# Kernel tuning notes

Measured on AMD Instinct MI355X. Metric: run time of the kernel, lower is better.

## Reference

```python
import jax, jax.numpy as jnp
import numpy as np

N_NODES = 50000


def _gcn_conv(x, W, b, src, dst, n):
    # PyG GCNConv: linear, then D^{-1/2}(A+I)D^{-1/2} aggregation, then bias.
    x = x @ W  # [N, out]
    loops = jnp.arange(n, dtype=src.dtype)
    src_f = jnp.concatenate([src, loops])  # add self-loops
    dst_f = jnp.concatenate([dst, loops])
    deg = jax.ops.segment_sum(jnp.ones_like(dst_f, dtype=x.dtype), dst_f, num_segments=n)
    dinv = jnp.where(deg > 0, jax.lax.rsqrt(deg), 0.0)
    norm = dinv[src_f] * dinv[dst_f]            # [E+N]
    msg = x[src_f] * norm[:, None]              # gather + scale
    out = jax.ops.segment_sum(msg, dst_f, num_segments=n)  # scatter-add
    return out + b


def setup_inputs() -> dict:
    key = jax.random.key(0)
    k1, k2, k3, k4 = jax.random.split(key, 4)
    ninp = 128
    emb = jax.random.normal(k1, (N_NODES, ninp), dtype=jnp.float32)
    emb = emb.at[0].set(0.0)  # padding_idx=0
    W1 = jax.random.normal(k2, (ninp, 2 * ninp), dtype=jnp.float32) * (1.0 / np.sqrt(ninp))
    b1 = jnp.zeros((2 * ninp,), dtype=jnp.float32)
    W2 = jax.random.normal(k3, (2 * ninp, ninp), dtype=jnp.float32) * (1.0 / np.sqrt(2 * ninp))
    b2 = jnp.zeros((ninp,), dtype=jnp.float32)
    edge_index = jax.random.randint(k4, (2, 800000), 0, N_NODES, dtype=jnp.int64)
    return {"emb": emb, "W1": W1, "b1": b1, "W2": W2, "b2": b2, "edge_index": edge_index}


def reference(emb, W1, b1, W2, b2, edge_index) -> jnp.ndarray:
    src, dst = edge_index[0], edge_index[1]
    h = _gcn_conv(emb, W1, b1, src, dst, N_NODES)   # [N, 2*ninp]
    # dropout in eval mode -> identity
    out = _gcn_conv(h, W2, b2, src, dst, N_NODES)   # [N, ninp]
    return out
```

## Files before the change

kernel.cpp:

```cpp
#include <hip/hip_runtime.h>

#define N_NODES 50000
#define N_EDGES 800000
#define NB 196

typedef unsigned int uint;
typedef short bf16x8 __attribute__((ext_vector_type(8)));
typedef float f32x4 __attribute__((ext_vector_type(4)));
typedef uint uint4v __attribute__((ext_vector_type(4)));

__device__ __forceinline__ ushort f2bf(float f) {
    union { float f; uint u; } v; v.f = f;
    uint r = (v.u + 0x7FFFu + ((v.u >> 16) & 1u)) >> 16;
    return (ushort)r;
}
__device__ __forceinline__ float bf_lo(uint u) { return __uint_as_float(u << 16); }
__device__ __forceinline__ float bf_hi(uint u) { return __uint_as_float(u & 0xFFFF0000u); }

__global__ void k_prep(const float* __restrict__ emb, const float* __restrict__ W1,
                       const float* __restrict__ W2, const float* __restrict__ b1,
                       uint* __restrict__ emb_h, ushort* __restrict__ W12t,
                       float* __restrict__ bvec, int* __restrict__ counts) {
    int b = blockIdx.x;
    int tid = threadIdx.x;
    if (b < 3125) {
        int t = b * 256 + tid;
        const float4* i4 = (const float4*)emb + (size_t)t * 2;
        float4 v0 = i4[0], v1 = i4[1];
        uint4 o;
        o.x = (uint)f2bf(v0.x) | ((uint)f2bf(v0.y) << 16);
        o.y = (uint)f2bf(v0.z) | ((uint)f2bf(v0.w) << 16);
        o.z = (uint)f2bf(v1.x) | ((uint)f2bf(v1.y) << 16);
        o.w = (uint)f2bf(v1.z) | ((uint)f2bf(v1.w) << 16);
        ((uint4*)emb_h)[t] = o;
    } else if (b < 3125 + NB) {
        int i = (b - 3125) * 256 + tid;
        if (i < N_NODES) counts[i] = 0;
    } else {
        int k = (b - (3125 + NB)) * 2 + (tid >> 7);
        int n = tid & 127;
        float s = 0.f;
        if (k < 128) {
            for (int m = 0; m < 256; ++m) s = fmaf(W1[(size_t)k * 256 + m], W2[(size_t)m * 128 + n], s);
            W12t[(size_t)n * 128 + k] = f2bf(s);
        } else if (k == 128) {
            for (int m = 0; m < 256; ++m) s = fmaf(b1[m], W2[(size_t)m * 128 + n], s);
            bvec[n] = s;
        }
    }
}


__global__ void k_histrank(const int* __restrict__ dst, int* __restrict__ counts,
                           ushort* __restrict__ rank) {
    int e = blockIdx.x * 256 + threadIdx.x;
    if (e < N_EDGES) rank[e] = (ushort)atomicAdd(&counts[dst[e]], 1);
}

__global__ void k_blocksum(const int* __restrict__ counts, int* __restrict__ bsum) {
    __shared__ int lds[256];
    int t = threadIdx.x;
    int i = blockIdx.x * 256 + t;
    int v = (i < N_NODES) ? counts[i] : 0;
    lds[t] = v;
    __syncthreads();
    for (int off = 128; off > 0; off >>= 1) {
        if (t < off) lds[t] += lds[t + off];
        __syncthreads();
    }
    if (t == 0) bsum[blockIdx.x] = lds[0];
}

__global__ void k_scanb(const int* __restrict__ bsum, int* __restrict__ boff) {
    __shared__ int lds[256];
    int t = threadIdx.x;
    int v = (t < NB) ? bsum[t] : 0;
    lds[t] = v;
    __syncthreads();
    for (int off = 1; off < 256; off <<= 1) {
        int o = (t >= off) ? lds[t - off] : 0;
        __syncthreads();
        lds[t] += o;
        __syncthreads();
    }
    if (t < NB) boff[t] = lds[t] - v;
}

__global__ void k_scatter_rp(const int* __restrict__ counts, const int* __restrict__ boff,
                             int* __restrict__ row_ptr, float* __restrict__ dinv) {
    __shared__ int lds[256];
    int t = threadIdx.x;
    int i = blockIdx.x * 256 + t;
    int v = (i < N_NODES) ? counts[i] : 0;
    lds[t] = v;
    __syncthreads();
    for (int off = 1; off < 256; off <<= 1) {
        int o = (t >= off) ? lds[t - off] : 0;
        __syncthreads();
        lds[t] += o;
        __syncthreads();
    }
    if (i < N_NODES) {
        row_ptr[i] = boff[blockIdx.x] + lds[t] - v;
        dinv[i] = rsqrtf((float)(v + 1));
    }
    if (i == 0) row_ptr[N_NODES] = N_EDGES;
}

__global__ void k_fillr(const int* __restrict__ src, const int* __restrict__ dst,
                        const ushort* __restrict__ rank, const int* __restrict__ row_ptr,
                        const float* __restrict__ dinv, uint* __restrict__ csr) {
    int e = blockIdx.x * 256 + threadIdx.x;
    if (e >= N_EDGES) return;
    int s = src[e];
    int pos = row_ptr[dst[e]] + (int)rank[e];
    csr[pos] = ((uint)s << 16) | (uint)f2bf(dinv[s]);
}

__device__ __forceinline__ void gather_core(const uint* __restrict__ xh,
                                            const uint* __restrict__ csr,
                                            int beg, int end, int node, float dd,
                                            int q, int fl, float o[8], float& scn) {
    const uint4* xb = (const uint4*)xh;
    float a[8];
    #pragma unroll
    for (int i = 0; i < 8; ++i) a[i] = 0.f;
    float sc = 0.f;

    for (int j = beg + q; j < end; j += 32) {
        uint e0 = csr[j];
        uint def = e0 & 0xFFFF0000u;
        uint e[8];
        e[0] = e0;
        #pragma unroll
        for (int i = 1; i < 8; ++i) {
            int ji = j + 4 * i;
            e[i] = (ji < end) ? csr[ji] : def;
        }
        uint4 u[8];
        #pragma unroll
        for (int i = 0; i < 8; ++i) u[i] = xb[(size_t)(e[i] >> 16) * 16 + fl];
        #pragma unroll
        for (int i = 0; i < 8; ++i) {
            float c = bf_lo(e[i]);
            sc += c;
            a[0] = fmaf(c, bf_lo(u[i].x), a[0]); a[1] = fmaf(c, bf_hi(u[i].x), a[1]);
            a[2] = fmaf(c, bf_lo(u[i].y), a[2]); a[3] = fmaf(c, bf_hi(u[i].y), a[3]);
            a[4] = fmaf(c, bf_lo(u[i].z), a[4]); a[5] = fmaf(c, bf_hi(u[i].z), a[5]);
            a[6] = fmaf(c, bf_lo(u[i].w), a[6]); a[7] = fmaf(c, bf_hi(u[i].w), a[7]);
        }
    }
    #pragma unroll
    for (int off = 16; off < 64; off <<= 1) {
        #pragma unroll
        for (int i = 0; i < 8; ++i) a[i] += __shfl_xor(a[i], off);
        sc += __shfl_xor(sc, off);
    }
    float dd2 = dd * dd;
    const uint4* xs = (const uint4*)xh + (size_t)node * 16 + fl;
    uint4 u = *xs;
    float s[8] = { bf_lo(u.x), bf_hi(u.x), bf_lo(u.y), bf_hi(u.y),
                   bf_lo(u.z), bf_hi(u.z), bf_lo(u.w), bf_hi(u.w) };
    #pragma unroll
    for (int i = 0; i < 8; ++i) o[i] = fmaf(dd, a[i], dd2 * s[i]);
    scn = fmaf(dd, sc, dd2);
}

__global__ void k_gather1(const uint* __restrict__ xh, const uint* __restrict__ csr,
                          const int* __restrict__ rp, const float* __restrict__ dinv,
                          uint* __restrict__ outp) {
    int node = blockIdx.x * 4 + (threadIdx.x >> 6);
    int lane = threadIdx.x & 63;
    int q = lane >> 4, fl = lane & 15;
    int beg = rp[node], end = rp[node + 1];
    float o[8], scn;
    gather_core(xh, csr, beg, end, node, dinv[node], q, fl, o, scn);
    if (q == 0) {
        uint4v p;
        p.x = (uint)f2bf(o[0]) | ((uint)f2bf(o[1]) << 16);
        p.y = (uint)f2bf(o[2]) | ((uint)f2bf(o[3]) << 16);
        p.z = (uint)f2bf(o[4]) | ((uint)f2bf(o[5]) << 16);
        p.w = (uint)f2bf(o[6]) | ((uint)f2bf(o[7]) << 16);
        __builtin_nontemporal_store(p, (uint4v*)outp + (size_t)node * 16 + fl);
    }
}

__global__ void __launch_bounds__(1024)
k_gather_gemm(const uint* __restrict__ xh, const uint* __restrict__ csr,
              const int* __restrict__ rp, const float* __restrict__ dinv,
              const ushort* __restrict__ Wt, const float* __restrict__ bvec,
              const float* __restrict__ b2, float* __restrict__ out) {
    __shared__ ushort rows[16 * 128];
    __shared__ float nvl[16];
    const int w = threadIdx.x >> 6;
    const int lane = threadIdx.x & 63;
    const int node = blockIdx.x * 16 + w;
    const int q = lane >> 4, fl = lane & 15;
    const int beg = rp[node], end = rp[node + 1];

    float o[8], scn;
    gather_core(xh, csr, beg, end, node, dinv[node], q, fl, o, scn);
    if (q == 0) {
        uint4 p;
        p.x = (uint)f2bf(o[0]) | ((uint)f2bf(o[1]) << 16);
        p.y = (uint)f2bf(o[2]) | ((uint)f2bf(o[3]) << 16);
        p.z = (uint)f2bf(o[4]) | ((uint)f2bf(o[5]) << 16);
        p.w = (uint)f2bf(o[6]) | ((uint)f2bf(o[7]) << 16);
        int idx = (w * 128 + fl * 8) ^ ((w & 7) << 3);
        *(uint4*)&rows[idx] = p;
        if (fl == 0) nvl[w] = scn;
    }
    __syncthreads();

    if (w < 8) {
        const int col = w * 16 + (lane & 15);
        const int ksub = (lane >> 4) * 8;
        const int row = lane & 15;
        f32x4 acc = (f32x4){0.f, 0.f, 0.f, 0.f};
        #pragma unroll
        for (int kc = 0; kc < 4; ++kc) {
            int idxr = (row * 128 + kc * 32 + ksub) ^ ((row & 7) << 3);
            bf16x8 af = *(const bf16x8*)&rows[idxr];
            bf16x8 bf = *(const bf16x8*)(Wt + (size_t)col * 128 + kc * 32 + ksub);
            acc = __builtin_amdgcn_mfma_f32_16x16x32_bf16(af, bf, acc, 0, 0, 0);
        }
        const int rb = (lane >> 4) * 4;
        float bv = bvec[col], bb = b2[col];
        #pragma unroll
        for (int e = 0; e < 4; ++e) {
            float nv = nvl[rb + e];
            out[(size_t)(blockIdx.x * 16 + rb + e) * 128 + col] = acc[e] + nv * bv + bb;
        }
    }
}

extern "C" void kernel_launch(void* const* d_in, const int* in_sizes, int n_in,
                              void* d_out, int out_size, void* d_ws, size_t ws_size,
                              hipStream_t stream) {
    const float* emb = (const float*)d_in[0];
    const float* W1  = (const float*)d_in[1];
    const float* b1  = (const float*)d_in[2];
    const float* W2  = (const float*)d_in[3];
    const float* b2  = (const float*)d_in[4];
    const int*   ei  = (const int*)d_in[5];
    const int* src = ei;
    const int* dst = ei + N_EDGES;

    char* ws = (char*)d_ws;
    float*  dinv    = (float*) (ws);
    int*    counts  = (int*)   (ws + (256ull << 10));
    int*    row_ptr = (int*)   (ws + (512ull << 10));
    int*    bsum    = (int*)   (ws + (768ull << 10));
    int*    boff    = (int*)   (ws + (772ull << 10));
    ushort* rank    = (ushort*)(ws + (1ull << 20));
    uint*   csr     = (uint*)  (ws + (3ull << 20));
    ushort* W12t    = (ushort*)(ws + (6656ull << 10));
    float*  bvec    = (float*) (ws + (6720ull << 10));
    uint*   emb_h   = (uint*)  (ws + (7ull  << 20));
    uint*   G       = (uint*)  (ws + (20ull << 20));
    float*  out     = (float*)d_out;

    k_prep<<<3386, 256, 0, stream>>>(emb, W1, W2, b1, emb_h, W12t, bvec, counts);

    k_histrank<<<(N_EDGES + 255) / 256, 256, 0, stream>>>(dst, counts, rank);
    k_blocksum<<<NB, 256, 0, stream>>>(counts, bsum);
    k_scanb<<<1, 256, 0, stream>>>(bsum, boff);
    k_scatter_rp<<<NB, 256, 0, stream>>>(counts, boff, row_ptr, dinv);
    k_fillr<<<(N_EDGES + 255) / 256, 256, 0, stream>>>(src, dst, rank, row_ptr, dinv, csr);

    k_gather1<<<12500, 256, 0, stream>>>(emb_h, csr, row_ptr, dinv, G);
    k_gather_gemm<<<3125, 1024, 0, stream>>>(G, csr, row_ptr, dinv,
                                             (const ushort*)W12t, bvec, b2, out);
}
```

Baseline: 171.5 us.

## Split fused second gather+GEMM into separate gather and MFMA GEMM kernels

Replaces the fused 1024-thread gather+GEMM kernel with a 256-thread gather kernel that writes bf16 aggregated rows and a per-node scale to workspace, followed by a separate MFMA GEMM kernel. The aim is to free the gather from the block-wide barrier and idle waves of the fused kernel, which should improve occupancy. It also marks CSR loads as nontemporal. The cost is an extra kernel launch and an extra round trip of the intermediate through global memory.

```diff
diff --git a/kernel.cpp b/kernel.cpp
--- a/kernel.cpp
+++ b/kernel.cpp
@@ -128,14 +128,14 @@
     float sc = 0.f;
 
     for (int j = beg + q; j < end; j += 32) {
-        uint e0 = csr[j];
+        uint e0 = __builtin_nontemporal_load(&csr[j]);
         uint def = e0 & 0xFFFF0000u;
         uint e[8];
         e[0] = e0;
         #pragma unroll
         for (int i = 1; i < 8; ++i) {
             int ji = j + 4 * i;
-            e[i] = (ji < end) ? csr[ji] : def;
+            e[i] = (ji < end) ? __builtin_nontemporal_load(&csr[ji]) : def;
         }
         uint4 u[8];
         #pragma unroll
@@ -185,51 +185,64 @@
     }
 }
 
-__global__ void __launch_bounds__(1024)
-k_gather_gemm(const uint* __restrict__ xh, const uint* __restrict__ csr,
-              const int* __restrict__ rp, const float* __restrict__ dinv,
-              const ushort* __restrict__ Wt, const float* __restrict__ bvec,
-              const float* __restrict__ b2, float* __restrict__ out) {
-    __shared__ ushort rows[16 * 128];
-    __shared__ float nvl[16];
-    const int w = threadIdx.x >> 6;
-    const int lane = threadIdx.x & 63;
-    const int node = blockIdx.x * 16 + w;
-    const int q = lane >> 4, fl = lane & 15;
-    const int beg = rp[node], end = rp[node + 1];
-
+__global__ void k_gather2(const uint* __restrict__ xh, const uint* __restrict__ csr,
+                          const int* __restrict__ rp, const float* __restrict__ dinv,
+                          uint* __restrict__ outp, float* __restrict__ nvec) {
+    int node = blockIdx.x * 4 + (threadIdx.x >> 6);
+    int lane = threadIdx.x & 63;
+    int q = lane >> 4, fl = lane & 15;
+    int beg = rp[node], end = rp[node + 1];
     float o[8], scn;
     gather_core(xh, csr, beg, end, node, dinv[node], q, fl, o, scn);
     if (q == 0) {
-        uint4 p;
+        uint4v p;
         p.x = (uint)f2bf(o[0]) | ((uint)f2bf(o[1]) << 16);
         p.y = (uint)f2bf(o[2]) | ((uint)f2bf(o[3]) << 16);
         p.z = (uint)f2bf(o[4]) | ((uint)f2bf(o[5]) << 16);
         p.w = (uint)f2bf(o[6]) | ((uint)f2bf(o[7]) << 16);
-        int idx = (w * 128 + fl * 8) ^ ((w & 7) << 3);
-        *(uint4*)&rows[idx] = p;
-        if (fl == 0) nvl[w] = scn;
-    }
-    __syncthreads();
-
-    if (w < 8) {
-        const int col = w * 16 + (lane & 15);
-        const int ksub = (lane >> 4) * 8;
-        const int row = lane & 15;
-        f32x4 acc = (f32x4){0.f, 0.f, 0.f, 0.f};
-        #pragma unroll
-        for (int kc = 0; kc < 4; ++kc) {
-            int idxr = (row * 128 + kc * 32 + ksub) ^ ((row & 7) << 3);
-            bf16x8 af = *(const bf16x8*)&rows[idxr];
-            bf16x8 bf = *(const bf16x8*)(Wt + (size_t)col * 128 + kc * 32 + ksub);
-            acc = __builtin_amdgcn_mfma_f32_16x16x32_bf16(af, bf, acc, 0, 0, 0);
-        }
-        const int rb = (lane >> 4) * 4;
-        float bv = bvec[col], bb = b2[col];
+        __builtin_nontemporal_store(p, (uint4v*)outp + (size_t)node * 16 + fl);
+        if (fl == 0) nvec[node] = scn;
+    }
+}
+
+__global__ void __launch_bounds__(256)
+k_gemm_out(const ushort* __restrict__ A, const ushort* __restrict__ Wt,
+           const float* __restrict__ nvec, const float* __restrict__ bvec,
+           const float* __restrict__ b2, float* __restrict__ out) {
+    constexpr int K = 128, NC = 128, KC = 4, TPW = 2;
+    const int lane = threadIdx.x & 63;
+    const int wave = threadIdx.x >> 6;
+    const int row0 = blockIdx.x * 16;
+    const int r = row0 + (lane & 15);
+    const int ksub = (lane >> 4) * 8;
+
+    f32x4 acc[TPW];
+    int col[TPW];
+    #pragma unroll
+    for (int t = 0; t < TPW; ++t) {
+        acc[t] = (f32x4){0.f, 0.f, 0.f, 0.f};
+        col[t] = (wave * TPW + t) * 16 + (lane & 15);
+    }
+    #pragma unroll
+    for (int kc = 0; kc < KC; ++kc) {
+        bf16x8 af = *(const bf16x8*)(A + (size_t)r * K + kc * 32 + ksub);
+        #pragma unroll
+        for (int t = 0; t < TPW; ++t) {
+            bf16x8 bf = *(const bf16x8*)(Wt + (size_t)col[t] * K + kc * 32 + ksub);
+            acc[t] = __builtin_amdgcn_mfma_f32_16x16x32_bf16(af, bf, acc[t], 0, 0, 0);
+        }
+    }
+    const int rb = row0 + (lane >> 4) * 4;
+    float nv[4];
+    #pragma unroll
+    for (int e = 0; e < 4; ++e) nv[e] = nvec[rb + e];
+    #pragma unroll
+    for (int t = 0; t < TPW; ++t) {
+        float bv = bvec[col[t]];
+        float bb = b2[col[t]];
         #pragma unroll
         for (int e = 0; e < 4; ++e) {
-            float nv = nvl[rb + e];
-            out[(size_t)(blockIdx.x * 16 + rb + e) * 128 + col] = acc[e] + nv * bv + bb;
+            out[(size_t)(rb + e) * NC + col[t]] = acc[t][e] + nv[e] * bv + bb;
         }
     }
 }
@@ -256,8 +269,10 @@
     uint*   csr     = (uint*)  (ws + (3ull << 20));
     ushort* W12t    = (ushort*)(ws + (6656ull << 10));
     float*  bvec    = (float*) (ws + (6720ull << 10));
+    float*  nvec    = (float*) (ws + (6784ull << 10));
     uint*   emb_h   = (uint*)  (ws + (7ull  << 20));
     uint*   G       = (uint*)  (ws + (20ull << 20));
+    uint*   G2      = (uint*)  (ws + (33ull << 20));
     float*  out     = (float*)d_out;
 
     k_prep<<<3386, 256, 0, stream>>>(emb, W1, W2, b1, emb_h, W12t, bvec, counts);
@@ -269,6 +284,6 @@
     k_fillr<<<(N_EDGES + 255) / 256, 256, 0, stream>>>(src, dst, rank, row_ptr, dinv, csr);
 
     k_gather1<<<12500, 256, 0, stream>>>(emb_h, csr, row_ptr, dinv, G);
-    k_gather_gemm<<<3125, 1024, 0, stream>>>(G, csr, row_ptr, dinv,
-                                             (const ushort*)W12t, bvec, b2, out);
-}
+    k_gather2<<<12500, 256, 0, stream>>>(G, csr, row_ptr, dinv, G2, nvec);
+    k_gemm_out<<<N_NODES / 16, 256, 0, stream>>>((const ushort*)G2, W12t, nvec, bvec, b2, out);
+}
```

Result: no change. 174.6 us (+1.8%).
